# Optimization experiments

Hardware: AMD Instinct MI355X
Metric: run time of the kernel (lower is better)

The kernel has to match this reference:

```python
import jax, jax.numpy as jnp
import numpy as np

N = 4096        # num_queries == gnn_query_dim
C1 = 1001       # classes + 1
D = 4096        # gnn_query_dim
H_MLP = 1024    # mlp_hidden_dim
H = 256         # hidden_dim
O = 256         # output_dim
TOP_K = 32
BN_EPS = 1e-5


def setup_inputs() -> dict:
    key = jax.random.key(0)
    ks = jax.random.split(key, 14)
    def lin(kw, fan_in, shape):
        s = 1.0 / np.sqrt(fan_in)
        return jax.random.uniform(kw, shape, jnp.float32, -s, s)
    return {
        "probs": jax.random.uniform(ks[0], (N, C1), jnp.float32),
        "bbox_coords": jax.random.uniform(ks[1], (N, 4), jnp.float32),
        "query_emb": jax.random.normal(ks[2], (N, D), jnp.float32) * 0.02,
        "node_emb": jax.random.normal(ks[3], (N, D), jnp.float32) * 0.02,
        "mlp_w1": lin(ks[4], D + 4 + C1, (D + 4 + C1, H_MLP)),
        "mlp_b1": lin(ks[5], D + 4 + C1, (H_MLP,)),
        "mlp_w2": lin(ks[6], H_MLP, (H_MLP, N)),
        "mlp_b2": lin(ks[7], H_MLP, (N,)),
        "conv_w1": lin(ks[8], D, (D, H)),
        "conv_b1": lin(ks[9], D, (H,)),
        "conv_w2": lin(ks[10], H, (H, O)),
        "conv_b2": lin(ks[11], H, (O,)),
        "bn_gamma": jnp.ones((H,), jnp.float32),
        "bn_beta": jnp.zeros((H,), jnp.float32),
    }


def reference(probs, bbox_coords, query_emb, node_emb,
              mlp_w1, mlp_b1, mlp_w2, mlp_b2,
              conv_w1, conv_b1, conv_w2, conv_b2,
              bn_gamma, bn_beta):
    # edge-weight MLP -> dense dynamic adjacency logits (N, N)
    ew_in = jnp.concatenate([query_emb, probs, bbox_coords], axis=-1)
    h = jax.nn.relu(ew_in @ mlp_w1 + mlp_b1)
    adj = h @ mlp_w2 + mlp_b2                      # (N, N)

    # top-k neighbors per node (sparse dynamic graph)
    vals, idx = jax.lax.top_k(adj, TOP_K)          # (N, K), (N, K)

    # GCN symmetric normalization from row-degree (sum of top-k weights)
    deg = jnp.sum(vals, axis=-1)                   # (N,)
    dinv = jnp.where(deg > 0, jax.lax.rsqrt(jnp.maximum(deg, 1e-12)), 0.0)
    wn = vals * dinv[:, None] * dinv[idx]          # (N, K)

    def gcn_conv(x, w, b):
        # gather neighbor features, weighted sum, then linear
        msg = jnp.einsum('nk,nkf->nf', wn, x[idx])  # (N, F)
        return msg @ w + b

    out = gcn_conv(node_emb, conv_w1, conv_b1)      # (N, H)
    # BatchNorm1d (batch statistics, training-mode math)
    mean = jnp.mean(out, axis=0)
    var = jnp.var(out, axis=0)
    out = (out - mean) * jax.lax.rsqrt(var + BN_EPS) * bn_gamma + bn_beta
    out = jax.nn.relu(out)
    # dropout is identity in eval mode
    out = gcn_conv(out, conv_w2, conv_b2)           # (N, O)
    return out
```

## Files before the change

### kernel.cpp

```cpp
#include <hip/hip_runtime.h>
#include <cfloat>

#define N_NODES 4096
#define C1_DIM  1001
#define D_DIM   4096
#define HMLP    1024
#define KCAT    (D_DIM + C1_DIM + 4)
#define K1PAD   5120
#define TOPK    32

typedef unsigned short u16;
typedef __bf16 bf16x8 __attribute__((ext_vector_type(8)));
typedef float  f32x4  __attribute__((ext_vector_type(4)));

__device__ __forceinline__ unsigned rne_bits(float x) {
  const unsigned u = __float_as_uint(x);
  return u + 0x7FFFu + ((u >> 16) & 1u);
}

__device__ __forceinline__ void gload16(const void* g, void* l) {
  __builtin_amdgcn_global_load_lds(
      (const __attribute__((address_space(1))) unsigned int*)g,
      (__attribute__((address_space(3))) unsigned int*)l, 16, 0, 0);
}

__global__ __launch_bounds__(256) void split_q(
    const float* __restrict__ in, u16* __restrict__ hi, u16* __restrict__ lo) {
  const size_t idx = ((size_t)blockIdx.x * 256 + threadIdx.x) * 8;
  const int row = (int)(idx >> 12);
  const int col = (int)(idx & 4095);
  const float4 x0 = *(const float4*)(in + idx);
  const float4 x1 = *(const float4*)(in + idx + 4);
  const float xs[8] = {x0.x, x0.y, x0.z, x0.w, x1.x, x1.y, x1.z, x1.w};
  unsigned hw[4], lw[4];
#pragma unroll
  for (int p = 0; p < 4; ++p) {
    const unsigned v0 = rne_bits(xs[2*p]);
    const unsigned v1 = rne_bits(xs[2*p+1]);
    hw[p] = (v1 & 0xFFFF0000u) | (v0 >> 16);
    const float r0 = xs[2*p]   - __uint_as_float(v0 & 0xFFFF0000u);
    const float r1 = xs[2*p+1] - __uint_as_float(v1 & 0xFFFF0000u);
    lw[p] = (rne_bits(r1) & 0xFFFF0000u) | (rne_bits(r0) >> 16);
  }
  const size_t o = (size_t)row * K1PAD + col;
  *(uint4*)(hi + o) = make_uint4(hw[0], hw[1], hw[2], hw[3]);
  *(uint4*)(lo + o) = make_uint4(lw[0], lw[1], lw[2], lw[3]);
}

__global__ __launch_bounds__(256) void tail_split(
    const float* __restrict__ probs, const float* __restrict__ bbox,
    u16* __restrict__ hi, u16* __restrict__ lo) {
  const int i = blockIdx.x * 256 + threadIdx.x;
  const int n = i >> 10, c = i & 1023;
  float v = 0.f;
  if (c < C1_DIM)          v = probs[n * C1_DIM + c];
  else if (c < C1_DIM + 4) v = bbox[n * 4 + (c - C1_DIM)];
  const unsigned vh = rne_bits(v);
  const float r = v - __uint_as_float(vh & 0xFFFF0000u);
  const size_t o = (size_t)n * K1PAD + D_DIM + c;
  hi[o] = (u16)(vh >> 16);
  lo[o] = (u16)(rne_bits(r) >> 16);
}

__global__ __launch_bounds__(256) void transpose_split(
    const float* __restrict__ in, int R, int C, int Rpad,
    u16* __restrict__ out_hi, u16* __restrict__ out_lo) {
  __shared__ float t[64][65];
  const int rb = blockIdx.x * 64;
  const int cb = blockIdx.y * 64;
  const int tid = threadIdx.x;
  const int lr = tid >> 6, lc = tid & 63;
#pragma unroll
  for (int i = 0; i < 16; ++i) {
    const int r = lr + i * 4;
    const int gr = rb + r;
    t[r][lc] = (gr < R) ? in[(size_t)gr * C + cb + lc] : 0.f;
  }
  __syncthreads();
#pragma unroll
  for (int i = 0; i < 16; ++i) {
    const int c = lr + i * 4;
    const float v = t[lc][c];
    const unsigned vh = rne_bits(v);
    const float r = v - __uint_as_float(vh & 0xFFFF0000u);
    const size_t o = (size_t)(cb + c) * Rpad + rb + lc;
    out_hi[o] = (u16)(vh >> 16);
    out_lo[o] = (u16)(rne_bits(r) >> 16);
  }
}


template<bool RELU, bool OUT_SPLIT, bool HASBIAS>
__device__ __forceinline__ void epilogue_64(
    f32x4 (&acc)[4][2], int row0, int col0, int wr0, int wc0, int lane,
    const float* bias, float* Cf, u16* Chi, u16* Clo, int N) {
#pragma unroll
  for (int mi = 0; mi < 4; ++mi)
#pragma unroll
    for (int ni = 0; ni < 2; ++ni) {
      const int gcol = col0 + wc0 + ni * 16 + (lane & 15);
      const float b = HASBIAS ? bias[gcol] : 0.f;
#pragma unroll
      for (int r = 0; r < 4; ++r) {
        const int grow = row0 + wr0 + mi * 16 + (lane >> 4) * 4 + r;
        float v = acc[mi][ni][r] + b;
        if (RELU) v = fmaxf(v, 0.f);
        if (OUT_SPLIT) {
          const unsigned vh = rne_bits(v);
          Chi[(size_t)grow * N + gcol] = (u16)(vh >> 16);
          const float rr = v - __uint_as_float(vh & 0xFFFF0000u);
          Clo[(size_t)grow * N + gcol] = (u16)(rne_bits(rr) >> 16);
        } else {
          Cf[(size_t)grow * N + gcol] = v;
        }
      }
    }
}

template<bool RELU, bool OUT_SPLIT, bool HASBIAS>
__device__ __forceinline__ void gemm_pipe3(
    int bx, int by,
    const u16* __restrict__ Ahi, const u16* __restrict__ Alo, int lda,
    const u16* __restrict__ Bthi, const u16* __restrict__ Btlo, int ldb,
    const float* __restrict__ bias,
    float* __restrict__ Cf, u16* __restrict__ Chi, u16* __restrict__ Clo,
    int N, int K, u16* lds) {
  const int tid = threadIdx.x;
  const int lane = tid & 63, wave = tid >> 6;
  const int row0 = by * 128, col0 = bx * 64;
  const int wr0 = (wave >> 1) * 64, wc0 = (wave & 1) * 32;
  const int srow = tid >> 2;
  const int sk   = ((tid & 3) ^ ((tid >> 3) & 3)) * 8;
  const int wu   = (tid & ~63) * 8;

  f32x4 acc[4][2];
#pragma unroll
  for (int mi = 0; mi < 4; ++mi)
#pragma unroll
    for (int ni = 0; ni < 2; ++ni) acc[mi][ni] = (f32x4){0.f, 0.f, 0.f, 0.f};

  auto stage = [&](int buf, int k0) {
    u16* base = lds + buf * 12288;
    gload16(Ahi + (size_t)(row0 + srow) * lda + k0 + sk,      base + wu);
    gload16(Ahi + (size_t)(row0 + 64 + srow) * lda + k0 + sk, base + 2048 + wu);
    gload16(Alo + (size_t)(row0 + srow) * lda + k0 + sk,      base + 4096 + wu);
    gload16(Alo + (size_t)(row0 + 64 + srow) * lda + k0 + sk, base + 6144 + wu);
    gload16(Bthi + (size_t)(col0 + srow) * ldb + k0 + sk, base + 8192 + wu);
    gload16(Btlo + (size_t)(col0 + srow) * ldb + k0 + sk, base + 10240 + wu);
  };
  auto compute = [&](int buf) {
    u16* base = lds + buf * 12288;
    const int ko_swz = ((lane >> 4) ^ ((lane >> 1) & 3)) * 8;
    const int ar = lane & 15;
    bf16x8 ah[4], al[4], bh[2], bl[2];
#pragma unroll
    for (int mi = 0; mi < 4; ++mi) {
      const int r = wr0 + mi * 16 + ar;
      ah[mi] = *(const bf16x8*)&base[r * 32 + ko_swz];
      al[mi] = *(const bf16x8*)&base[4096 + r * 32 + ko_swz];
    }
#pragma unroll
    for (int ni = 0; ni < 2; ++ni) {
      const int c = wc0 + ni * 16 + ar;
      bh[ni] = *(const bf16x8*)&base[8192 + c * 32 + ko_swz];
      bl[ni] = *(const bf16x8*)&base[10240 + c * 32 + ko_swz];
    }
#pragma unroll
    for (int mi = 0; mi < 4; ++mi)
#pragma unroll
      for (int ni = 0; ni < 2; ++ni) {
        acc[mi][ni] = __builtin_amdgcn_mfma_f32_16x16x32_bf16(ah[mi], bh[ni], acc[mi][ni], 0, 0, 0);
        acc[mi][ni] = __builtin_amdgcn_mfma_f32_16x16x32_bf16(ah[mi], bl[ni], acc[mi][ni], 0, 0, 0);
        acc[mi][ni] = __builtin_amdgcn_mfma_f32_16x16x32_bf16(al[mi], bh[ni], acc[mi][ni], 0, 0, 0);
      }
  };

  const int nk = K >> 5;
  stage(0, 0);
  stage(1, 32);
  int cb = 0;
  for (int k = 0; k < nk; ++k) {
    if (k + 2 < nk) {
      int sb = cb + 2; if (sb >= 3) sb -= 3;
      stage(sb, (k + 2) * 32);
      asm volatile("s_waitcnt vmcnt(12)" ::: "memory");
    } else if (k + 1 < nk) {
      asm volatile("s_waitcnt vmcnt(6)" ::: "memory");
    } else {
      asm volatile("s_waitcnt vmcnt(0)" ::: "memory");
    }
    __builtin_amdgcn_s_barrier();
    compute(cb);
    __builtin_amdgcn_s_barrier();
    ++cb; if (cb >= 3) cb -= 3;
  }

  epilogue_64<RELU, OUT_SPLIT, HASBIAS>(acc, row0, col0, wr0, wc0, lane,
                                        bias, Cf, Chi, Clo, N);
}

template<bool HASBIAS>
__device__ __forceinline__ void gemm_pipe128(
    int bx, int by,
    const u16* __restrict__ Ahi, const u16* __restrict__ Alo, int lda,
    const u16* __restrict__ Bthi, const u16* __restrict__ Btlo, int ldb,
    const float* __restrict__ bias, float* __restrict__ Cf,
    int N, int K, u16* lds) {
  const int tid = threadIdx.x;
  const int lane = tid & 63, wave = tid >> 6;
  const int row0 = by * 128, col0 = bx * 128;
  const int wr0 = (wave >> 1) * 64, wc0 = (wave & 1) * 64;
  const int srow = tid >> 2;
  const int sk   = ((tid & 3) ^ ((tid >> 3) & 3)) * 8;
  const int wu   = (tid & ~63) * 8;

  f32x4 acc[4][4];
#pragma unroll
  for (int mi = 0; mi < 4; ++mi)
#pragma unroll
    for (int ni = 0; ni < 4; ++ni) acc[mi][ni] = (f32x4){0.f, 0.f, 0.f, 0.f};

  auto stage = [&](int buf, int k0) {
    u16* base = lds + buf * 16384;
    gload16(Ahi + (size_t)(row0 + srow) * lda + k0 + sk,      base + wu);
    gload16(Ahi + (size_t)(row0 + 64 + srow) * lda + k0 + sk, base + 2048 + wu);
    gload16(Alo + (size_t)(row0 + srow) * lda + k0 + sk,      base + 4096 + wu);
    gload16(Alo + (size_t)(row0 + 64 + srow) * lda + k0 + sk, base + 6144 + wu);
    gload16(Bthi + (size_t)(col0 + srow) * ldb + k0 + sk,      base + 8192 + wu);
    gload16(Bthi + (size_t)(col0 + 64 + srow) * ldb + k0 + sk, base + 10240 + wu);
    gload16(Btlo + (size_t)(col0 + srow) * ldb + k0 + sk,      base + 12288 + wu);
    gload16(Btlo + (size_t)(col0 + 64 + srow) * ldb + k0 + sk, base + 14336 + wu);
  };
  auto compute = [&](int buf) {
    u16* base = lds + buf * 16384;
    const int ko_swz = ((lane >> 4) ^ ((lane >> 1) & 3)) * 8;
    const int ar = lane & 15;
    bf16x8 ah[4], al[4], bh[4], bl[4];
#pragma unroll
    for (int mi = 0; mi < 4; ++mi) {
      const int r = wr0 + mi * 16 + ar;
      ah[mi] = *(const bf16x8*)&base[r * 32 + ko_swz];
      al[mi] = *(const bf16x8*)&base[4096 + r * 32 + ko_swz];
    }
#pragma unroll
    for (int ni = 0; ni < 4; ++ni) {
      const int c = wc0 + ni * 16 + ar;
      bh[ni] = *(const bf16x8*)&base[8192 + c * 32 + ko_swz];
      bl[ni] = *(const bf16x8*)&base[12288 + c * 32 + ko_swz];
    }
#pragma unroll
    for (int mi = 0; mi < 4; ++mi)
#pragma unroll
      for (int ni = 0; ni < 4; ++ni) {
        acc[mi][ni] = __builtin_amdgcn_mfma_f32_16x16x32_bf16(ah[mi], bh[ni], acc[mi][ni], 0, 0, 0);
        acc[mi][ni] = __builtin_amdgcn_mfma_f32_16x16x32_bf16(ah[mi], bl[ni], acc[mi][ni], 0, 0, 0);
        acc[mi][ni] = __builtin_amdgcn_mfma_f32_16x16x32_bf16(al[mi], bh[ni], acc[mi][ni], 0, 0, 0);
      }
  };

  const int nk = K >> 5;
  stage(0, 0);
  int cur = 0;
  for (int k = 0; k < nk; ++k) {
    if (k + 1 < nk) {
      stage(cur ^ 1, (k + 1) * 32);
      asm volatile("s_waitcnt vmcnt(8)" ::: "memory");
    } else {
      asm volatile("s_waitcnt vmcnt(0)" ::: "memory");
    }
    __builtin_amdgcn_s_barrier();
    compute(cur);
    __builtin_amdgcn_s_barrier();
    cur ^= 1;
  }

#pragma unroll
  for (int mi = 0; mi < 4; ++mi)
#pragma unroll
    for (int ni = 0; ni < 4; ++ni) {
      const int gcol = col0 + wc0 + ni * 16 + (lane & 15);
      const float b = HASBIAS ? bias[gcol] : 0.f;
#pragma unroll
      for (int r = 0; r < 4; ++r) {
        const int grow = row0 + wr0 + mi * 16 + (lane >> 4) * 4 + r;
        Cf[(size_t)grow * N + gcol] = acc[mi][ni][r] + b;
      }
    }
}

template<bool RELU, bool OUT_SPLIT, bool HASBIAS>
__device__ __forceinline__ void gemm_a1(
    int bx, int by,
    const float* __restrict__ Aq,
    const u16* __restrict__ Bthi, const u16* __restrict__ Btlo, int ldb,
    const float* __restrict__ bias,
    float* __restrict__ Cf, u16* __restrict__ Chi, u16* __restrict__ Clo,
    int N, int K, u16* lds) {
  const int tid = threadIdx.x;
  const int lane = tid & 63, wave = tid >> 6;
  const int row0 = by * 128, col0 = bx * 64;
  const int wr0 = (wave >> 1) * 64, wc0 = (wave & 1) * 32;
  const int srow = tid >> 2, skof = (tid & 3) * 8;
  const int sk   = ((tid & 3) ^ ((tid >> 3) & 3)) * 8;
  const int wu = (tid & ~63) * 8;

  f32x4 acc[4][2];
#pragma unroll
  for (int mi = 0; mi < 4; ++mi)
#pragma unroll
    for (int ni = 0; ni < 2; ++ni) acc[mi][ni] = (f32x4){0.f, 0.f, 0.f, 0.f};

  auto stageB = [&](int buf, int k0) {
    u16* base = lds + buf * 12288;
    gload16(Bthi + (size_t)(col0 + srow) * ldb + k0 + sk, base + 8192 + wu);
    gload16(Btlo + (size_t)(col0 + srow) * ldb + k0 + sk, base + 10240 + wu);
  };
  auto loadA1 = [&](int k0, float4* x) {
    const int kk = k0 + skof;
#pragma unroll
    for (int j = 0; j < 2; ++j) {
      const int grow = row0 + srow + j * 64;
      const float* src = Aq + (size_t)grow * D_DIM + kk;
      x[j * 2]     = *(const float4*)src;
      x[j * 2 + 1] = *(const float4*)(src + 4);
    }
  };
  auto writeA1 = [&](int buf, const float4* x) {
    u16* base = lds + buf * 12288;
#pragma unroll
    for (int j = 0; j < 2; ++j) {
      const float xs[8] = {x[j*2].x, x[j*2].y, x[j*2].z, x[j*2].w,
                           x[j*2+1].x, x[j*2+1].y, x[j*2+1].z, x[j*2+1].w};
      unsigned hw[4], lw[4];
#pragma unroll
      for (int p = 0; p < 4; ++p) {
        const unsigned v0 = rne_bits(xs[2*p]);
        const unsigned v1 = rne_bits(xs[2*p+1]);
        hw[p] = (v1 & 0xFFFF0000u) | (v0 >> 16);
        const float r0 = xs[2*p]   - __uint_as_float(v0 & 0xFFFF0000u);
        const float r1 = xs[2*p+1] - __uint_as_float(v1 & 0xFFFF0000u);
        lw[p] = (rne_bits(r1) & 0xFFFF0000u) | (rne_bits(r0) >> 16);
      }
      *(uint4*)&base[(srow + j * 64) * 32 + sk] = make_uint4(hw[0], hw[1], hw[2], hw[3]);
      *(uint4*)&base[4096 + (srow + j * 64) * 32 + sk] = make_uint4(lw[0], lw[1], lw[2], lw[3]);
    }
  };
  auto compute = [&](int buf) {
    u16* base = lds + buf * 12288;
    const int ko_swz = ((lane >> 4) ^ ((lane >> 1) & 3)) * 8;
    const int ar = lane & 15;
    bf16x8 ah[4], al[4], bh[2], bl[2];
#pragma unroll
    for (int mi = 0; mi < 4; ++mi) {
      const int r = wr0 + mi * 16 + ar;
      ah[mi] = *(const bf16x8*)&base[r * 32 + ko_swz];
      al[mi] = *(const bf16x8*)&base[4096 + r * 32 + ko_swz];
    }
#pragma unroll
    for (int ni = 0; ni < 2; ++ni) {
      const int c = wc0 + ni * 16 + ar;
      bh[ni] = *(const bf16x8*)&base[8192 + c * 32 + ko_swz];
      bl[ni] = *(const bf16x8*)&base[10240 + c * 32 + ko_swz];
    }
#pragma unroll
    for (int mi = 0; mi < 4; ++mi)
#pragma unroll
      for (int ni = 0; ni < 2; ++ni) {
        acc[mi][ni] = __builtin_amdgcn_mfma_f32_16x16x32_bf16(ah[mi], bh[ni], acc[mi][ni], 0, 0, 0);
        acc[mi][ni] = __builtin_amdgcn_mfma_f32_16x16x32_bf16(ah[mi], bl[ni], acc[mi][ni], 0, 0, 0);
        acc[mi][ni] = __builtin_amdgcn_mfma_f32_16x16x32_bf16(al[mi], bh[ni], acc[mi][ni], 0, 0, 0);
      }
  };

  int cur = 0;
  float4 x[4];
  loadA1(0, x); stageB(0, 0); writeA1(0, x);
  __syncthreads();
  for (int k0 = 0; k0 < K; k0 += 32) {
    const bool nx = (k0 + 32 < K);
    float4 xn[4];
    if (nx) { loadA1(k0 + 32, xn); stageB(cur ^ 1, k0 + 32); }
    compute(cur);
    if (nx) writeA1(cur ^ 1, xn);
    __syncthreads();
    cur ^= 1;
  }

  epilogue_64<RELU, OUT_SPLIT, HASBIAS>(acc, row0, col0, wr0, wc0, lane,
                                        bias, Cf, Chi, Clo, N);
}

__global__ __launch_bounds__(256, 2) void gemm1_kernel(
    const u16* __restrict__ a_hi, const u16* __restrict__ a_lo,
    const u16* __restrict__ w1t_hi, const u16* __restrict__ w1t_lo,
    const float* __restrict__ b1,
    u16* __restrict__ h_hi, u16* __restrict__ h_lo) {
  __shared__ u16 lds[3 * 12288];
  gemm_pipe3<true, true, true>(blockIdx.x, blockIdx.y,
      a_hi, a_lo, K1PAD, w1t_hi, w1t_lo, K1PAD, b1,
      nullptr, h_hi, h_lo, HMLP, K1PAD, lds);
}

__global__ __launch_bounds__(256, 2) void fused2_kernel(
    const u16* __restrict__ h_hi, const u16* __restrict__ h_lo,
    const u16* __restrict__ w2t_hi, const u16* __restrict__ w2t_lo,
    const float* __restrict__ b2, float* __restrict__ adj,
    const float* __restrict__ node,
    const u16* __restrict__ w1ct_hi, const u16* __restrict__ w1ct_lo,
    float* __restrict__ Z1) {
  __shared__ u16 lds[2 * 16384];
  const int bid = blockIdx.x;
  if (bid < 128) {
    gemm_a1<false, false, false>(bid & 3, bid >> 2,
        node, w1ct_hi, w1ct_lo, D_DIM, nullptr,
        Z1, nullptr, nullptr, 256, D_DIM, lds);
  } else {
    const int r = bid - 128;
    gemm_pipe128<true>(r & 31, r >> 5,
        h_hi, h_lo, HMLP, w2t_hi, w2t_lo, HMLP, b2,
        adj, N_NODES, HMLP, lds);
  }
}

__global__ __launch_bounds__(256) void gemm_small(
    const float* __restrict__ A, const float* __restrict__ B,
    float* __restrict__ C, int M, int Ncols, int K) {
  __shared__ float As[16][68];
  __shared__ float Bs[16][68];
  const int tid = threadIdx.x;
  const int row0 = blockIdx.y * 64, col0 = blockIdx.x * 64;
  const int tx = tid & 15, ty = tid >> 4;
  const int arow = tid >> 2, acol = (tid & 3) * 4;
  const int brow = tid >> 4, bcol = (tid & 15) * 4;

  float acc[4][4];
#pragma unroll
  for (int i = 0; i < 4; ++i)
#pragma unroll
    for (int j = 0; j < 4; ++j) acc[i][j] = 0.f;

  for (int k0 = 0; k0 < K; k0 += 16) {
    const float4 a4 = *(const float4*)(A + (size_t)(row0 + arow) * K + k0 + acol);
    const float4 b4 = *(const float4*)(B + (size_t)(k0 + brow) * Ncols + col0 + bcol);
    __syncthreads();
    As[acol + 0][arow] = a4.x; As[acol + 1][arow] = a4.y;
    As[acol + 2][arow] = a4.z; As[acol + 3][arow] = a4.w;
    *(float4*)&Bs[brow][bcol] = b4;
    __syncthreads();
#pragma unroll
    for (int k = 0; k < 16; ++k) {
      float av[4], bw[4];
      *(float4*)&av[0] = *(const float4*)&As[k][ty * 4];
      *(float4*)&bw[0] = *(const float4*)&Bs[k][tx * 4];
#pragma unroll
      for (int i = 0; i < 4; ++i)
#pragma unroll
        for (int j = 0; j < 4; ++j) acc[i][j] += av[i] * bw[j];
    }
  }

#pragma unroll
  for (int i = 0; i < 4; ++i) {
    const int r = row0 + ty * 4 + i;
    float4 v;
    v.x = acc[i][0]; v.y = acc[i][1]; v.z = acc[i][2]; v.w = acc[i][3];
    *(float4*)(C + (size_t)r * Ncols + col0 + tx * 4) = v;
  }
}

__global__ __launch_bounds__(256) void topk_kernel(
    const float* __restrict__ adj, float* __restrict__ vals,
    int* __restrict__ idxo, float* __restrict__ dinv) {
  __shared__ float sv[N_NODES];
  __shared__ float rw[4];
  __shared__ int   iw[4];
  const int n = blockIdx.x, tid = threadIdx.x;
  const int lane = tid & 63, wave = tid >> 6;
  const float4* rowp = (const float4*)(adj + (size_t)n * N_NODES);

  float mv = -FLT_MAX; int mi = 0x7FFFFFFF;
  for (int g = tid; g < N_NODES / 4; g += 256) {
    const float4 v4 = rowp[g];
    *(float4*)&sv[g * 4] = v4;
    if (v4.x > mv) { mv = v4.x; mi = g * 4 + 0; }
    if (v4.y > mv) { mv = v4.y; mi = g * 4 + 1; }
    if (v4.z > mv) { mv = v4.z; mi = g * 4 + 2; }
    if (v4.w > mv) { mv = v4.w; mi = g * 4 + 3; }
  }

  float sum = 0.f;
  for (int it = 0; it < TOPK; ++it) {
    float bv = mv; int bi = mi;
#pragma unroll
    for (int off = 1; off < 64; off <<= 1) {
      const float ov = __shfl_xor(bv, off);
      const int   oi = __shfl_xor(bi, off);
      if (ov > bv || (ov == bv && oi < bi)) { bv = ov; bi = oi; }
    }
    if (lane == 0) { rw[wave] = bv; iw[wave] = bi; }
    __syncthreads();
    bv = rw[0]; bi = iw[0];
#pragma unroll
    for (int w = 1; w < 4; ++w) {
      const float ov = rw[w]; const int oi = iw[w];
      if (ov > bv || (ov == bv && oi < bi)) { bv = ov; bi = oi; }
    }
    if (tid == 0) {
      vals[(size_t)n * TOPK + it] = bv;
      idxo[(size_t)n * TOPK + it] = bi;
    }
    sum += bv;
    if (tid == ((bi >> 2) & 255)) {
      sv[bi] = -FLT_MAX;
      mv = -FLT_MAX; mi = 0x7FFFFFFF;
      for (int g = tid; g < N_NODES / 4; g += 256) {
#pragma unroll
        for (int e = 0; e < 4; ++e) {
          const float v = sv[g * 4 + e];
          if (v > mv) { mv = v; mi = g * 4 + e; }
        }
      }
    }
    __syncthreads();
  }
  if (tid == 0)
    dinv[n] = (sum > 0.f) ? rsqrtf(fmaxf(sum, 1e-12f)) : 0.f;
}

__global__ __launch_bounds__(256) void agg_kernel(
    const float* __restrict__ Z, const float* __restrict__ vals,
    const int* __restrict__ idxo, const float* __restrict__ dinv,
    const float* __restrict__ bias, float* __restrict__ out) {
  const int n = blockIdx.x, f = threadIdx.x;
  const float dn = dinv[n];
  float acc = bias[f];
#pragma unroll
  for (int k = 0; k < TOPK; ++k) {
    const int   j = idxo[n * TOPK + k];
    const float w = vals[n * TOPK + k] * dn * dinv[j];
    acc += w * Z[(size_t)j * 256 + f];
  }
  out[(size_t)n * 256 + f] = acc;
}

__global__ __launch_bounds__(256) void bn_partial(
    const float* __restrict__ x, float* __restrict__ partial) {
  const int b = blockIdx.x, c = threadIdx.x;
  float s = 0.f, s2 = 0.f;
  for (int r = b * 32; r < b * 32 + 32; ++r) {
    const float v = x[(size_t)r * 256 + c];
    s += v; s2 += v * v;
  }
  partial[(size_t)b * 512 + c]       = s;
  partial[(size_t)b * 512 + 256 + c] = s2;
}

__global__ __launch_bounds__(256) void bn_reduce(
    const float* __restrict__ partial, float* __restrict__ colstats) {
  const int j = blockIdx.x, t = threadIdx.x;
  __shared__ float red[128];
  if (t < 128) red[t] = partial[(size_t)t * 512 + j];
  __syncthreads();
  for (int s = 64; s > 0; s >>= 1) {
    if (t < s) red[t] += red[t + s];
    __syncthreads();
  }
  if (t == 0) colstats[j] = red[0];
}

__global__ __launch_bounds__(256) void bn_apply(
    float* __restrict__ x, const float* __restrict__ colstats,
    const float* __restrict__ gamma, const float* __restrict__ beta) {
  const int i = blockIdx.x * 256 + threadIdx.x;
  const int c = i & 255;
  const float mean = colstats[c] * (1.f / 4096.f);
  float var = colstats[256 + c] * (1.f / 4096.f) - mean * mean;
  var = fmaxf(var, 0.f);
  const float v = (x[i] - mean) * rsqrtf(var + 1e-5f) * gamma[c] + beta[c];
  x[i] = fmaxf(v, 0.f);
}

extern "C" void kernel_launch(void* const* d_in, const int* in_sizes, int n_in,
                              void* d_out, int out_size, void* d_ws, size_t ws_size,
                              hipStream_t stream) {
  const float* probs   = (const float*)d_in[0];
  const float* bbox    = (const float*)d_in[1];
  const float* query   = (const float*)d_in[2];
  const float* node    = (const float*)d_in[3];
  const float* mlp_w1  = (const float*)d_in[4];
  const float* mlp_b1  = (const float*)d_in[5];
  const float* mlp_w2  = (const float*)d_in[6];
  const float* mlp_b2  = (const float*)d_in[7];
  const float* conv_w1 = (const float*)d_in[8];
  const float* conv_b1 = (const float*)d_in[9];
  const float* conv_w2 = (const float*)d_in[10];
  const float* conv_b2 = (const float*)d_in[11];
  const float* gamma   = (const float*)d_in[12];
  const float* beta    = (const float*)d_in[13];

  float* ws = (float*)d_ws;
  size_t off = 0;
  float* R1 = ws + off;  off += (size_t)N_NODES * K1PAD;
  u16* a_hi = (u16*)R1;
  u16* a_lo = a_hi + (size_t)N_NODES * K1PAD;
  float* adj = R1;
  float* spare = R1 + (size_t)N_NODES * N_NODES;
  float* Z1   = spare;
  float* vals = spare + (size_t)N_NODES * 256;
  int*   idxo = (int*)(vals + (size_t)N_NODES * TOPK);
  float* dinv = (float*)idxo + (size_t)N_NODES * TOPK;
  float* partial  = dinv + N_NODES;
  float* colstats = partial + 128 * 512;
  float* R2 = ws + off;  off += (size_t)HMLP * K1PAD;
  u16* w1t_hi = (u16*)R2;
  u16* w1t_lo = w1t_hi + (size_t)HMLP * K1PAD;
  u16* w2t_hi = (u16*)R2;
  u16* w2t_lo = w2t_hi + (size_t)N_NODES * HMLP;
  u16* w1ct_hi = (u16*)(R2 + (size_t)N_NODES * HMLP);
  u16* w1ct_lo = w1ct_hi + (size_t)256 * D_DIM;
  float* out1 = R2 + (size_t)N_NODES * HMLP;
  float* R3 = ws + off;  off += (size_t)N_NODES * HMLP;
  u16* h_hi = (u16*)R3;
  u16* h_lo = h_hi + (size_t)N_NODES * HMLP;
  float* Z2 = adj;

  split_q<<<(N_NODES * D_DIM) / (256 * 8), 256, 0, stream>>>(query, a_hi, a_lo);
  tail_split<<<(N_NODES * 1024) / 256, 256, 0, stream>>>(probs, bbox, a_hi, a_lo);
  transpose_split<<<dim3(K1PAD / 64, HMLP / 64), 256, 0, stream>>>(
      mlp_w1, KCAT, HMLP, K1PAD, w1t_hi, w1t_lo);
  gemm1_kernel<<<dim3(HMLP / 64, N_NODES / 128), 256, 0, stream>>>(
      a_hi, a_lo, w1t_hi, w1t_lo, mlp_b1, h_hi, h_lo);
  transpose_split<<<dim3(HMLP / 64, N_NODES / 64), 256, 0, stream>>>(
      mlp_w2, HMLP, N_NODES, HMLP, w2t_hi, w2t_lo);
  transpose_split<<<dim3(D_DIM / 64, 256 / 64), 256, 0, stream>>>(
      conv_w1, D_DIM, 256, D_DIM, w1ct_hi, w1ct_lo);
  fused2_kernel<<<128 + (N_NODES / 128) * (N_NODES / 128), 256, 0, stream>>>(
      h_hi, h_lo, w2t_hi, w2t_lo, mlp_b2, adj, node, w1ct_hi, w1ct_lo, Z1);
  topk_kernel<<<N_NODES, 256, 0, stream>>>(adj, vals, idxo, dinv);
  agg_kernel<<<N_NODES, 256, 0, stream>>>(Z1, vals, idxo, dinv, conv_b1, out1);
  bn_partial<<<128, 256, 0, stream>>>(out1, partial);
  bn_reduce<<<512, 256, 0, stream>>>(partial, colstats);
  bn_apply<<<N_NODES, 256, 0, stream>>>(out1, colstats, gamma, beta);
  gemm_small<<<dim3(256 / 64, N_NODES / 64), 256, 0, stream>>>(
      out1, conv_w2, Z2, N_NODES, 256, 256);
  agg_kernel<<<N_NODES, 256, 0, stream>>>(Z2, vals, idxo, dinv, conv_b2, (float*)d_out);
}
```

Before: 603.4 us.

## Stage fp32 node features via async LDS loads with triple-buffered pipeline

Replaces the register-staged, double-buffered A-operand path in the node-feature GEMM with direct global-to-LDS async loads of raw fp32 tiles in a three-stage pipeline. The bf16 hi/lo split now happens at fragment-read time from LDS instead of before the LDS write. The aim is to hide global latency and drop the VGPR round trip, at the cost of repeating the split conversion per wave read. The adjacency GEMM block indices are also remapped so that concurrently running blocks share A-row tiles for better L2 reuse. LDS use grows to three 12288-element buffers.

```diff
diff --git a/kernel.cpp b/kernel.cpp
--- a/kernel.cpp
+++ b/kernel.cpp
@@ -197,6 +197,102 @@
 
   epilogue_64<RELU, OUT_SPLIT, HASBIAS>(acc, row0, col0, wr0, wc0, lane,
                                         bias, Cf, Chi, Clo, N);
+}
+
+__device__ __forceinline__ void gemm_a1p(
+    int bx, int by,
+    const float* __restrict__ Aq, int lda,
+    const u16* __restrict__ Bthi, const u16* __restrict__ Btlo, int ldb,
+    float* __restrict__ Cf, int N, int K, u16* lds) {
+  const int tid = threadIdx.x;
+  const int lane = tid & 63, wave = tid >> 6;
+  const int row0 = by * 128, col0 = bx * 64;
+  const int wr0 = (wave >> 1) * 64, wc0 = (wave & 1) * 32;
+  const int srow = tid >> 2;
+  const int sk   = ((tid & 3) ^ ((tid >> 3) & 3)) * 8;
+  const int wu   = (tid & ~63) * 8;
+  const int arowA = tid >> 3;
+  const int skA   = ((tid & 7) ^ ((tid >> 3) & 7)) * 4;
+
+  f32x4 acc[4][2];
+#pragma unroll
+  for (int mi = 0; mi < 4; ++mi)
+#pragma unroll
+    for (int ni = 0; ni < 2; ++ni) acc[mi][ni] = (f32x4){0.f, 0.f, 0.f, 0.f};
+
+  auto stage = [&](int buf, int k0) {
+    u16* base = lds + buf * 12288;
+#pragma unroll
+    for (int j = 0; j < 4; ++j) {
+      gload16(Aq + (size_t)(row0 + 32 * j + arowA) * lda + k0 + skA,
+              base + j * 2048 + wu);
+    }
+    gload16(Bthi + (size_t)(col0 + srow) * ldb + k0 + sk, base + 8192 + wu);
+    gload16(Btlo + (size_t)(col0 + srow) * ldb + k0 + sk, base + 10240 + wu);
+  };
+  auto compute = [&](int buf) {
+    u16* base = lds + buf * 12288;
+    const float* Af = (const float*)base;
+    const int ko_swz = ((lane >> 4) ^ ((lane >> 1) & 3)) * 8;
+    const int c = lane >> 4;
+    const int ar = lane & 15;
+    bf16x8 ah[4], al[4], bh[2], bl[2];
+#pragma unroll
+    for (int mi = 0; mi < 4; ++mi) {
+      const int r = wr0 + mi * 16 + ar;
+      const int s = ar & 7;
+      const f32x4 a0 = *(const f32x4*)&Af[r * 32 + (((2 * c) ^ s) * 4)];
+      const f32x4 a1 = *(const f32x4*)&Af[r * 32 + (((2 * c + 1) ^ s) * 4)];
+      const float xs[8] = {a0[0], a0[1], a0[2], a0[3], a1[0], a1[1], a1[2], a1[3]};
+      union { u16 u[8]; bf16x8 v; } H, L;
+#pragma unroll
+      for (int e = 0; e < 8; ++e) {
+        const unsigned vh = rne_bits(xs[e]);
+        H.u[e] = (u16)(vh >> 16);
+        const float rr = xs[e] - __uint_as_float(vh & 0xFFFF0000u);
+        L.u[e] = (u16)(rne_bits(rr) >> 16);
+      }
+      ah[mi] = H.v; al[mi] = L.v;
+    }
+#pragma unroll
+    for (int ni = 0; ni < 2; ++ni) {
+      const int cc = wc0 + ni * 16 + ar;
+      bh[ni] = *(const bf16x8*)&base[8192 + cc * 32 + ko_swz];
+      bl[ni] = *(const bf16x8*)&base[10240 + cc * 32 + ko_swz];
+    }
+#pragma unroll
+    for (int mi = 0; mi < 4; ++mi)
+#pragma unroll
+      for (int ni = 0; ni < 2; ++ni) {
+        acc[mi][ni] = __builtin_amdgcn_mfma_f32_16x16x32_bf16(ah[mi], bh[ni], acc[mi][ni], 0, 0, 0);
+        acc[mi][ni] = __builtin_amdgcn_mfma_f32_16x16x32_bf16(ah[mi], bl[ni], acc[mi][ni], 0, 0, 0);
+        acc[mi][ni] = __builtin_amdgcn_mfma_f32_16x16x32_bf16(al[mi], bh[ni], acc[mi][ni], 0, 0, 0);
+      }
+  };
+
+  const int nk = K >> 5;
+  stage(0, 0);
+  stage(1, 32);
+  int cb = 0;
+  for (int k = 0; k < nk; ++k) {
+    if (k + 2 < nk) {
+      int sb = cb + 2; if (sb >= 3) sb -= 3;
+      stage(sb, (k + 2) * 32);
+      asm volatile("s_waitcnt vmcnt(12)" ::: "memory");
+    } else if (k + 1 < nk) {
+      asm volatile("s_waitcnt vmcnt(6)" ::: "memory");
+    } else {
+      asm volatile("s_waitcnt vmcnt(0)" ::: "memory");
+    }
+    __builtin_amdgcn_s_barrier();
+    compute(cb);
+    __builtin_amdgcn_s_barrier();
+    ++cb; if (cb >= 3) cb -= 3;
+  }
+
+  f32x4 (&accr)[4][2] = acc;
+  epilogue_64<false, false, false>(accr, row0, col0, wr0, wc0, lane,
+                                   nullptr, Cf, nullptr, nullptr, N);
 }
 
 template<bool HASBIAS>
@@ -288,108 +384,6 @@
     }
 }
 
-template<bool RELU, bool OUT_SPLIT, bool HASBIAS>
-__device__ __forceinline__ void gemm_a1(
-    int bx, int by,
-    const float* __restrict__ Aq,
-    const u16* __restrict__ Bthi, const u16* __restrict__ Btlo, int ldb,
-    const float* __restrict__ bias,
-    float* __restrict__ Cf, u16* __restrict__ Chi, u16* __restrict__ Clo,
-    int N, int K, u16* lds) {
-  const int tid = threadIdx.x;
-  const int lane = tid & 63, wave = tid >> 6;
-  const int row0 = by * 128, col0 = bx * 64;
-  const int wr0 = (wave >> 1) * 64, wc0 = (wave & 1) * 32;
-  const int srow = tid >> 2, skof = (tid & 3) * 8;
-  const int sk   = ((tid & 3) ^ ((tid >> 3) & 3)) * 8;
-  const int wu = (tid & ~63) * 8;
-
-  f32x4 acc[4][2];
-#pragma unroll
-  for (int mi = 0; mi < 4; ++mi)
-#pragma unroll
-    for (int ni = 0; ni < 2; ++ni) acc[mi][ni] = (f32x4){0.f, 0.f, 0.f, 0.f};
-
-  auto stageB = [&](int buf, int k0) {
-    u16* base = lds + buf * 12288;
-    gload16(Bthi + (size_t)(col0 + srow) * ldb + k0 + sk, base + 8192 + wu);
-    gload16(Btlo + (size_t)(col0 + srow) * ldb + k0 + sk, base + 10240 + wu);
-  };
-  auto loadA1 = [&](int k0, float4* x) {
-    const int kk = k0 + skof;
-#pragma unroll
-    for (int j = 0; j < 2; ++j) {
-      const int grow = row0 + srow + j * 64;
-      const float* src = Aq + (size_t)grow * D_DIM + kk;
-      x[j * 2]     = *(const float4*)src;
-      x[j * 2 + 1] = *(const float4*)(src + 4);
-    }
-  };
-  auto writeA1 = [&](int buf, const float4* x) {
-    u16* base = lds + buf * 12288;
-#pragma unroll
-    for (int j = 0; j < 2; ++j) {
-      const float xs[8] = {x[j*2].x, x[j*2].y, x[j*2].z, x[j*2].w,
-                           x[j*2+1].x, x[j*2+1].y, x[j*2+1].z, x[j*2+1].w};
-      unsigned hw[4], lw[4];
-#pragma unroll
-      for (int p = 0; p < 4; ++p) {
-        const unsigned v0 = rne_bits(xs[2*p]);
-        const unsigned v1 = rne_bits(xs[2*p+1]);
-        hw[p] = (v1 & 0xFFFF0000u) | (v0 >> 16);
-        const float r0 = xs[2*p]   - __uint_as_float(v0 & 0xFFFF0000u);
-        const float r1 = xs[2*p+1] - __uint_as_float(v1 & 0xFFFF0000u);
-        lw[p] = (rne_bits(r1) & 0xFFFF0000u) | (rne_bits(r0) >> 16);
-      }
-      *(uint4*)&base[(srow + j * 64) * 32 + sk] = make_uint4(hw[0], hw[1], hw[2], hw[3]);
-      *(uint4*)&base[4096 + (srow + j * 64) * 32 + sk] = make_uint4(lw[0], lw[1], lw[2], lw[3]);
-    }
-  };
-  auto compute = [&](int buf) {
-    u16* base = lds + buf * 12288;
-    const int ko_swz = ((lane >> 4) ^ ((lane >> 1) & 3)) * 8;
-    const int ar = lane & 15;
-    bf16x8 ah[4], al[4], bh[2], bl[2];
-#pragma unroll
-    for (int mi = 0; mi < 4; ++mi) {
-      const int r = wr0 + mi * 16 + ar;
-      ah[mi] = *(const bf16x8*)&base[r * 32 + ko_swz];
-      al[mi] = *(const bf16x8*)&base[4096 + r * 32 + ko_swz];
-    }
-#pragma unroll
-    for (int ni = 0; ni < 2; ++ni) {
-      const int c = wc0 + ni * 16 + ar;
-      bh[ni] = *(const bf16x8*)&base[8192 + c * 32 + ko_swz];
-      bl[ni] = *(const bf16x8*)&base[10240 + c * 32 + ko_swz];
-    }
-#pragma unroll
-    for (int mi = 0; mi < 4; ++mi)
-#pragma unroll
-      for (int ni = 0; ni < 2; ++ni) {
-        acc[mi][ni] = __builtin_amdgcn_mfma_f32_16x16x32_bf16(ah[mi], bh[ni], acc[mi][ni], 0, 0, 0);
-        acc[mi][ni] = __builtin_amdgcn_mfma_f32_16x16x32_bf16(ah[mi], bl[ni], acc[mi][ni], 0, 0, 0);
-        acc[mi][ni] = __builtin_amdgcn_mfma_f32_16x16x32_bf16(al[mi], bh[ni], acc[mi][ni], 0, 0, 0);
-      }
-  };
-
-  int cur = 0;
-  float4 x[4];
-  loadA1(0, x); stageB(0, 0); writeA1(0, x);
-  __syncthreads();
-  for (int k0 = 0; k0 < K; k0 += 32) {
-    const bool nx = (k0 + 32 < K);
-    float4 xn[4];
-    if (nx) { loadA1(k0 + 32, xn); stageB(cur ^ 1, k0 + 32); }
-    compute(cur);
-    if (nx) writeA1(cur ^ 1, xn);
-    __syncthreads();
-    cur ^= 1;
-  }
-
-  epilogue_64<RELU, OUT_SPLIT, HASBIAS>(acc, row0, col0, wr0, wc0, lane,
-                                        bias, Cf, Chi, Clo, N);
-}
-
 __global__ __launch_bounds__(256, 2) void gemm1_kernel(
     const u16* __restrict__ a_hi, const u16* __restrict__ a_lo,
     const u16* __restrict__ w1t_hi, const u16* __restrict__ w1t_lo,
@@ -408,15 +402,19 @@
     const float* __restrict__ node,
     const u16* __restrict__ w1ct_hi, const u16* __restrict__ w1ct_lo,
     float* __restrict__ Z1) {
-  __shared__ u16 lds[2 * 16384];
+  __shared__ u16 lds[3 * 12288];
   const int bid = blockIdx.x;
   if (bid < 128) {
-    gemm_a1<false, false, false>(bid & 3, bid >> 2,
-        node, w1ct_hi, w1ct_lo, D_DIM, nullptr,
-        Z1, nullptr, nullptr, 256, D_DIM, lds);
+    gemm_a1p(bid & 3, bid >> 2,
+             node, D_DIM, w1ct_hi, w1ct_lo, D_DIM,
+             Z1, 256, D_DIM, lds);
   } else {
     const int r = bid - 128;
-    gemm_pipe128<true>(r & 31, r >> 5,
+    const int x = r & 7;
+    const int i = r >> 3;
+    const int by = x * 4 + (i >> 5);
+    const int bx = i & 31;
+    gemm_pipe128<true>(bx, by,
         h_hi, h_lo, HMLP, w2t_hi, w2t_lo, HMLP, b2,
         adj, N_NODES, HMLP, lds);
   }
```

After: 568.7 us. 5.8% less time.
